# Kernel tuning notes

Hardware: AMD Instinct MI355X
Metric: run time of the kernel (lower is better)

The kernel has to match this reference:

```python
import jax, jax.numpy as jnp
import numpy as np

DIM = 4096
ROOT = 64  # int(sqrt(DIM))
B = 8192
LN_EPS = 1e-5


def setup_inputs() -> dict:
    key = jax.random.key(0)
    ks = jax.random.split(key, 7)
    return {
        "x": jax.random.normal(ks[0], (B, DIM), dtype=jnp.float32),
        "param_1": jax.random.normal(ks[1], (ROOT, 4 * ROOT, ROOT), dtype=jnp.float32),
        "bias_1": jax.random.normal(ks[2], (ROOT, 4 * ROOT), dtype=jnp.float32),
        "param_2": jax.random.normal(ks[3], (ROOT, ROOT, 4 * ROOT), dtype=jnp.float32),
        "bias_2": jax.random.normal(ks[4], (ROOT, ROOT), dtype=jnp.float32),
        "ln_gamma": jnp.ones((DIM,), dtype=jnp.float32),
        "ln_beta": jnp.zeros((DIM,), dtype=jnp.float32),
        "W": jax.random.normal(ks[5], (DIM, DIM), dtype=jnp.float32) * (1.0 / np.sqrt(DIM)),
        "b": jax.random.normal(ks[6], (DIM,), dtype=jnp.float32),
    }


def reference(x, param_1, bias_1, param_2, bias_2, ln_gamma, ln_beta, W, b):
    r = x
    # block-diagonal per-row matmuls: x -> [B, root, root]
    xb = x.reshape(-1, ROOT, ROOT)
    # fc_row: param_1[r] @ row + bias_1[r]  -> [B, root, 4*root]
    h = jnp.einsum("brk,rmk->brm", xb, param_1) + bias_1
    h = jax.nn.relu(h)
    # second per-row projection -> [B, root, root]
    h = jnp.einsum("brm,rkm->brk", h, param_2) + bias_2
    h = jax.nn.relu(h)
    h = h.reshape(-1, DIM)
    # LayerNorm (affine, eps=1e-5)
    mu = jnp.mean(h, axis=-1, keepdims=True)
    var = jnp.mean(jnp.square(h - mu), axis=-1, keepdims=True)
    h = (h - mu) * jax.lax.rsqrt(var + LN_EPS) * ln_gamma + ln_beta
    # Linear + ReLU + residual
    h = jax.nn.relu(h @ W.T + b)
    return h + r
```

## Files before the change

kernel.cpp:

```cpp
#include <hip/hip_runtime.h>

typedef __bf16 bf16;
typedef bf16 bf16x4 __attribute__((ext_vector_type(4)));
typedef bf16 bf16x8 __attribute__((ext_vector_type(8)));
typedef float floatx4 __attribute__((ext_vector_type(4)));

#define MFMA(a, b, c) __builtin_amdgcn_mfma_f32_16x16x32_bf16((a), (b), (c), 0, 0, 0)

__device__ __forceinline__ void gl2lds16(const void* g, void* l) {
  __builtin_amdgcn_global_load_lds(
      (const __attribute__((address_space(1))) void*)g,
      (__attribute__((address_space(3))) void*)l, 16, 0, 0);
}

__device__ __forceinline__ bf16x4 cvt4(const float4 v) {
  bf16x4 o;
  o[0] = (bf16)v.x; o[1] = (bf16)v.y; o[2] = (bf16)v.z; o[3] = (bf16)v.w;
  return o;
}

__global__ __launch_bounds__(256) void cast_w_kernel(const float* __restrict__ W,
                                                     bf16* __restrict__ Wb, int n4) {
  int idx = blockIdx.x * 256 + threadIdx.x;
  int stride = gridDim.x * 256;
  const float4* W4 = (const float4*)W;
  for (int i = idx; i < n4; i += stride) {
    *(bf16x4*)(Wb + (size_t)i * 4) = cvt4(W4[i]);
  }
}

__global__ __launch_bounds__(256) void blockdiag_kernel(
    const float* __restrict__ x, const float* __restrict__ p1,
    const float* __restrict__ b1, const float* __restrict__ p2,
    const float* __restrict__ b2, bf16* __restrict__ h2) {
  __shared__ bf16 sX[128 * 72];
  __shared__ bf16 sP1[64 * 72];
  __shared__ bf16 sP2[64 * 72];
  __shared__ bf16 sH1[128 * 72];
  __shared__ float sB1[256];
  __shared__ float sB2[64];

  const int tid = threadIdx.x;
  const int bt = blockIdx.x, r = blockIdx.y;
  const size_t b0 = (size_t)bt * 128;

  const float* xr = x + b0 * 4096 + r * 64;
#pragma unroll
  for (int i = 0; i < 8; ++i) {
    int idx = tid + i * 256;
    int row = idx >> 4, c4 = idx & 15;
    float4 v = *(const float4*)(xr + (size_t)row * 4096 + c4 * 4);
    *(bf16x4*)(&sX[row * 72 + c4 * 4]) = cvt4(v);
  }
  sB1[tid] = b1[r * 256 + tid];
  if (tid < 64) sB2[tid] = b2[r * 64 + tid];

  const float* p1r = p1 + (size_t)r * 16384;
  const float* p2r = p2 + (size_t)r * 16384;

  const int w = tid >> 6, lane = tid & 63;
  const int q = lane >> 4, l16 = lane & 15;
  const int wm = w >> 1, wn = w & 1;

  const floatx4 fzero = {0.f, 0.f, 0.f, 0.f};
  floatx4 acc2[4][2];
#pragma unroll
  for (int mt = 0; mt < 4; ++mt)
#pragma unroll
    for (int nt = 0; nt < 2; ++nt) acc2[mt][nt] = fzero;

  for (int qh = 0; qh < 4; ++qh) {
    __syncthreads();
#pragma unroll
    for (int i = 0; i < 4; ++i) {
      int idx = tid + i * 256;
      int row = idx >> 4, c4 = idx & 15;
      float4 v = *(const float4*)(p1r + (size_t)(qh * 64 + row) * 64 + c4 * 4);
      *(bf16x4*)(&sP1[row * 72 + c4 * 4]) = cvt4(v);
      float4 u = *(const float4*)(p2r + (size_t)row * 256 + qh * 64 + c4 * 4);
      *(bf16x4*)(&sP2[row * 72 + c4 * 4]) = cvt4(u);
    }
    __syncthreads();

    floatx4 acc1[4][2];
#pragma unroll
    for (int mt = 0; mt < 4; ++mt)
#pragma unroll
      for (int nt = 0; nt < 2; ++nt) acc1[mt][nt] = fzero;
#pragma unroll
    for (int ks = 0; ks < 2; ++ks) {
      bf16x8 a[4], bb[2];
#pragma unroll
      for (int mt = 0; mt < 4; ++mt)
        a[mt] = *(const bf16x8*)(&sX[(64 * wm + mt * 16 + l16) * 72 + ks * 32 + q * 8]);
#pragma unroll
      for (int nt = 0; nt < 2; ++nt)
        bb[nt] = *(const bf16x8*)(&sP1[(32 * wn + nt * 16 + l16) * 72 + ks * 32 + q * 8]);
#pragma unroll
      for (int mt = 0; mt < 4; ++mt)
#pragma unroll
        for (int nt = 0; nt < 2; ++nt) acc1[mt][nt] = MFMA(a[mt], bb[nt], acc1[mt][nt]);
    }
#pragma unroll
    for (int mt = 0; mt < 4; ++mt) {
#pragma unroll
      for (int nt = 0; nt < 2; ++nt) {
        int c = 32 * wn + nt * 16 + l16;
        float bias1v = sB1[qh * 64 + c];
#pragma unroll
        for (int v = 0; v < 4; ++v) {
          int row = 64 * wm + mt * 16 + q * 4 + v;
          sH1[row * 72 + c] = (bf16)fmaxf(acc1[mt][nt][v] + bias1v, 0.f);
        }
      }
    }
    __syncthreads();
#pragma unroll
    for (int ks = 0; ks < 2; ++ks) {
      bf16x8 a2[4], bb2[2];
#pragma unroll
      for (int mt = 0; mt < 4; ++mt)
        a2[mt] = *(const bf16x8*)(&sH1[(64 * wm + mt * 16 + l16) * 72 + ks * 32 + q * 8]);
#pragma unroll
      for (int nt = 0; nt < 2; ++nt)
        bb2[nt] = *(const bf16x8*)(&sP2[(32 * wn + nt * 16 + l16) * 72 + ks * 32 + q * 8]);
#pragma unroll
      for (int mt = 0; mt < 4; ++mt)
#pragma unroll
        for (int nt = 0; nt < 2; ++nt) acc2[mt][nt] = MFMA(a2[mt], bb2[nt], acc2[mt][nt]);
    }
  }

  bf16* ho = h2 + b0 * 4096 + r * 64;
#pragma unroll
  for (int mt = 0; mt < 4; ++mt) {
#pragma unroll
    for (int nt = 0; nt < 2; ++nt) {
      int kk = 32 * wn + nt * 16 + l16;
      float b2v = sB2[kk];
#pragma unroll
      for (int v = 0; v < 4; ++v) {
        int row = 64 * wm + mt * 16 + q * 4 + v;
        ho[(size_t)row * 4096 + kk] = (bf16)fmaxf(acc2[mt][nt][v] + b2v, 0.f);
      }
    }
  }
}

__global__ __launch_bounds__(256) void ln_kernel(bf16* __restrict__ h,
                                                 const float* __restrict__ gamma,
                                                 const float* __restrict__ beta) {
  const int row = blockIdx.x;
  const int tid = threadIdx.x;
  bf16* hr = h + (size_t)row * 4096;
  float vals[16];
  float s = 0.f, ss = 0.f;
#pragma unroll
  for (int i = 0; i < 2; ++i) {
    bf16x8 v = *(const bf16x8*)(hr + (size_t)(i * 256 + tid) * 8);
#pragma unroll
    for (int j = 0; j < 8; ++j) {
      float f = (float)v[j];
      vals[i * 8 + j] = f;
      s += f;
      ss += f * f;
    }
  }
#pragma unroll
  for (int off = 32; off > 0; off >>= 1) {
    s += __shfl_down(s, off, 64);
    ss += __shfl_down(ss, off, 64);
  }
  __shared__ float red[8];
  const int w = tid >> 6, lane = tid & 63;
  if (lane == 0) { red[w] = s; red[4 + w] = ss; }
  __syncthreads();
  s = red[0] + red[1] + red[2] + red[3];
  ss = red[4] + red[5] + red[6] + red[7];
  const float mu = s * (1.f / 4096.f);
  const float var = ss * (1.f / 4096.f) - mu * mu;
  const float rsig = rsqrtf(var + 1e-5f);
#pragma unroll
  for (int i = 0; i < 2; ++i) {
    const int base = (i * 256 + tid) * 8;
    float4 g0 = *(const float4*)(gamma + base);
    float4 g1 = *(const float4*)(gamma + base + 4);
    float4 be0 = *(const float4*)(beta + base);
    float4 be1 = *(const float4*)(beta + base + 4);
    float g[8] = {g0.x, g0.y, g0.z, g0.w, g1.x, g1.y, g1.z, g1.w};
    float bb[8] = {be0.x, be0.y, be0.z, be0.w, be1.x, be1.y, be1.z, be1.w};
    bf16x8 o;
#pragma unroll
    for (int j = 0; j < 8; ++j) o[j] = (bf16)((vals[i * 8 + j] - mu) * rsig * g[j] + bb[j]);
    *(bf16x8*)(hr + base) = o;
  }
}

__global__ __launch_bounds__(256) void gemm_kernel(
    const bf16* __restrict__ A,
    const bf16* __restrict__ B,
    const float* __restrict__ bias, const float* __restrict__ xres,
    float* __restrict__ out) {
  __shared__ bf16 sA[128 * 32];
  __shared__ bf16 sB[128 * 32];
  const int tid = threadIdx.x;
  const int n0 = blockIdx.x * 128;
  const int m0 = blockIdx.y * 128;
  const int w = tid >> 6, lane = tid & 63;
  const int q = lane >> 4, l16 = lane & 15;
  const int wm = w >> 1, wn = w & 1;

  const floatx4 fzero = {0.f, 0.f, 0.f, 0.f};
  floatx4 acc[4][4];
#pragma unroll
  for (int mt = 0; mt < 4; ++mt)
#pragma unroll
    for (int nt = 0; nt < 4; ++nt) acc[mt][nt] = fzero;

  const int ra = tid >> 2;
  const int koff = (tid & 3) * 8;
  const bf16* aptr = A + (size_t)(m0 + ra) * 4096 + koff;
  const bf16* bptr = B + (size_t)(n0 + ra) * 4096 + koff;
  bf16* la = sA + tid * 8;
  bf16* lb = sB + tid * 8;

  for (int k0 = 0; k0 < 4096; k0 += 32) {
    gl2lds16(aptr, la);
    gl2lds16(aptr + (size_t)64 * 4096, sA + 2048 + tid * 8);
    gl2lds16(bptr, lb);
    gl2lds16(bptr + (size_t)64 * 4096, sB + 2048 + tid * 8);
    aptr += 32;
    bptr += 32;
    __syncthreads();
    bf16x8 af[4], bfr[4];
#pragma unroll
    for (int mt = 0; mt < 4; ++mt)
      af[mt] = *(const bf16x8*)(&sA[(64 * wm + mt * 16 + l16) * 32 + q * 8]);
#pragma unroll
    for (int nt = 0; nt < 4; ++nt)
      bfr[nt] = *(const bf16x8*)(&sB[(64 * wn + nt * 16 + l16) * 32 + q * 8]);
#pragma unroll
    for (int mt = 0; mt < 4; ++mt)
#pragma unroll
      for (int nt = 0; nt < 4; ++nt) acc[mt][nt] = MFMA(af[mt], bfr[nt], acc[mt][nt]);
    __syncthreads();
  }

#pragma unroll
  for (int nt = 0; nt < 4; ++nt) {
    const int col = n0 + 64 * wn + nt * 16 + l16;
    const float bv = bias[col];
#pragma unroll
    for (int mt = 0; mt < 4; ++mt) {
#pragma unroll
      for (int v = 0; v < 4; ++v) {
        const int row = m0 + 64 * wm + mt * 16 + q * 4 + v;
        const size_t o = (size_t)row * 4096 + col;
        out[o] = fmaxf(acc[mt][nt][v] + bv, 0.f) + xres[o];
      }
    }
  }
}

extern "C" void kernel_launch(void* const* d_in, const int* in_sizes, int n_in,
                              void* d_out, int out_size, void* d_ws, size_t ws_size,
                              hipStream_t stream) {
  const float* x = (const float*)d_in[0];
  const float* p1 = (const float*)d_in[1];
  const float* b1 = (const float*)d_in[2];
  const float* p2 = (const float*)d_in[3];
  const float* b2 = (const float*)d_in[4];
  const float* gamma = (const float*)d_in[5];
  const float* beta = (const float*)d_in[6];
  const float* W = (const float*)d_in[7];
  const float* bias = (const float*)d_in[8];
  float* out = (float*)d_out;

  bf16* Wb = (bf16*)d_ws;
  bf16* h = (bf16*)((char*)d_ws + (size_t)4096 * 4096 * 2);

  cast_w_kernel<<<2048, 256, 0, stream>>>(W, Wb, 4096 * 4096 / 4);
  blockdiag_kernel<<<dim3(64, 64), 256, 0, stream>>>(x, p1, b1, p2, b2, h);
  ln_kernel<<<8192, 256, 0, stream>>>(h, gamma, beta);
  gemm_kernel<<<dim3(32, 64), 256, 0, stream>>>(h, Wb, bias, x, out);
}
```

Before: 746.9 us.

## Fold LayerNorm into GEMM epilogue, pre-cast inputs to bf16, swizzle LDS tiles

New measurement: 900.7 us. 20.6% more time.

```diff
diff --git a/kernel.cpp b/kernel.cpp
--- a/kernel.cpp
+++ b/kernel.cpp
@@ -19,23 +19,72 @@
   return o;
 }
 
-__global__ __launch_bounds__(256) void cast_w_kernel(const float* __restrict__ W,
-                                                     bf16* __restrict__ Wb, int n4) {
+__global__ __launch_bounds__(256) void castw_kernel(
+    const float* __restrict__ W, const float* __restrict__ gamma,
+    const float* __restrict__ beta, const float* __restrict__ bias,
+    bf16* __restrict__ Wb, float* __restrict__ g, float* __restrict__ cb) {
+  const int j = blockIdx.x, tid = threadIdx.x;
+  const float* wr = W + (size_t)j * 4096;
+  float wg = 0.f, wb = 0.f;
+  const int base = tid * 16;
+#pragma unroll
+  for (int i = 0; i < 4; ++i) {
+    float4 wv = *(const float4*)(wr + base + i * 4);
+    float4 gv = *(const float4*)(gamma + base + i * 4);
+    float4 bv = *(const float4*)(beta + base + i * 4);
+    float p0 = wv.x * gv.x, p1 = wv.y * gv.y, p2 = wv.z * gv.z, p3 = wv.w * gv.w;
+    bf16x4 o; o[0] = (bf16)p0; o[1] = (bf16)p1; o[2] = (bf16)p2; o[3] = (bf16)p3;
+    *(bf16x4*)(Wb + (size_t)j * 4096 + base + i * 4) = o;
+    wg += p0 + p1 + p2 + p3;
+    wb += wv.x * bv.x + wv.y * bv.y + wv.z * bv.z + wv.w * bv.w;
+  }
+#pragma unroll
+  for (int off = 32; off > 0; off >>= 1) {
+    wg += __shfl_down(wg, off, 64);
+    wb += __shfl_down(wb, off, 64);
+  }
+  __shared__ float red[8];
+  const int w = tid >> 6, lane = tid & 63;
+  if (lane == 0) { red[w] = wg; red[4 + w] = wb; }
+  __syncthreads();
+  if (tid == 0) {
+    g[j] = red[0] + red[1] + red[2] + red[3];
+    cb[j] = red[4] + red[5] + red[6] + red[7] + bias[j];
+  }
+}
+
+__global__ __launch_bounds__(256) void castx_kernel(const float* __restrict__ x,
+                                                    bf16* __restrict__ xb, int n4) {
   int idx = blockIdx.x * 256 + threadIdx.x;
   int stride = gridDim.x * 256;
-  const float4* W4 = (const float4*)W;
-  for (int i = idx; i < n4; i += stride) {
-    *(bf16x4*)(Wb + (size_t)i * 4) = cvt4(W4[i]);
+  const float4* x4 = (const float4*)x;
+  for (int i = idx; i < n4; i += stride) *(bf16x4*)(xb + (size_t)i * 4) = cvt4(x4[i]);
+}
+
+__global__ __launch_bounds__(256) void castp_kernel(const float* __restrict__ p1,
+                                                    const float* __restrict__ p2,
+                                                    bf16* __restrict__ p1b,
+                                                    bf16* __restrict__ p2b) {
+  int idx = blockIdx.x * 256 + threadIdx.x;
+  int stride = gridDim.x * 256;
+  const float4* a4 = (const float4*)p1;
+  const float4* b4 = (const float4*)p2;
+  for (int i = idx; i < 524288; i += stride) {
+    if (i < 262144) *(bf16x4*)(p1b + (size_t)i * 4) = cvt4(a4[i]);
+    else {
+      int k = i - 262144;
+      *(bf16x4*)(p2b + (size_t)k * 4) = cvt4(b4[k]);
+    }
   }
 }
 
 __global__ __launch_bounds__(256) void blockdiag_kernel(
-    const float* __restrict__ x, const float* __restrict__ p1,
-    const float* __restrict__ b1, const float* __restrict__ p2,
+    const bf16* __restrict__ xb, const bf16* __restrict__ p1b,
+    const float* __restrict__ b1, const bf16* __restrict__ p2b,
     const float* __restrict__ b2, bf16* __restrict__ h2) {
-  __shared__ bf16 sX[128 * 72];
-  __shared__ bf16 sP1[64 * 72];
-  __shared__ bf16 sP2[64 * 72];
+  __shared__ bf16 sX[128 * 64];
+  __shared__ bf16 sP1[64 * 64];
+  __shared__ bf16 sP2[64 * 64];
   __shared__ bf16 sH1[128 * 72];
   __shared__ float sB1[256];
   __shared__ float sB2[64];
@@ -44,24 +93,24 @@
   const int bt = blockIdx.x, r = blockIdx.y;
   const size_t b0 = (size_t)bt * 128;
 
-  const float* xr = x + b0 * 4096 + r * 64;
-#pragma unroll
-  for (int i = 0; i < 8; ++i) {
-    int idx = tid + i * 256;
-    int row = idx >> 4, c4 = idx & 15;
-    float4 v = *(const float4*)(xr + (size_t)row * 4096 + c4 * 4);
-    *(bf16x4*)(&sX[row * 72 + c4 * 4]) = cvt4(v);
+  const int srow = tid >> 3, ss = tid & 7;
+  const int sg = ss ^ (srow & 7);
+  {
+    const bf16* src = xb + (b0 + srow) * 4096 + r * 64 + sg * 8;
+#pragma unroll
+    for (int i = 0; i < 4; ++i)
+      gl2lds16(src + (size_t)i * 32 * 4096, sX + (tid + i * 256) * 8);
   }
   sB1[tid] = b1[r * 256 + tid];
   if (tid < 64) sB2[tid] = b2[r * 64 + tid];
-
-  const float* p1r = p1 + (size_t)r * 16384;
-  const float* p2r = p2 + (size_t)r * 16384;
 
   const int w = tid >> 6, lane = tid & 63;
   const int q = lane >> 4, l16 = lane & 15;
   const int wm = w >> 1, wn = w & 1;
 
+  const bf16* p1base = p1b + (size_t)r * 16384;
+  const bf16* p2base = p2b + (size_t)r * 16384;
+
   const floatx4 fzero = {0.f, 0.f, 0.f, 0.f};
   floatx4 acc2[4][2];
 #pragma unroll
@@ -70,17 +119,14 @@
     for (int nt = 0; nt < 2; ++nt) acc2[mt][nt] = fzero;
 
   for (int qh = 0; qh < 4; ++qh) {
+    if (qh) __syncthreads();
+#pragma unroll
+    for (int i = 0; i < 2; ++i) {
+      int row = srow + i * 32;
+      gl2lds16(p1base + (size_t)(qh * 64 + row) * 64 + sg * 8, sP1 + (tid + i * 256) * 8);
+      gl2lds16(p2base + (size_t)row * 256 + qh * 64 + sg * 8, sP2 + (tid + i * 256) * 8);
+    }
     __syncthreads();
-#pragma unroll
-    for (int i = 0; i < 4; ++i) {
-      int idx = tid + i * 256;
-      int row = idx >> 4, c4 = idx & 15;
-      float4 v = *(const float4*)(p1r + (size_t)(qh * 64 + row) * 64 + c4 * 4);
-      *(bf16x4*)(&sP1[row * 72 + c4 * 4]) = cvt4(v);
-      float4 u = *(const float4*)(p2r + (size_t)row * 256 + qh * 64 + c4 * 4);
-      *(bf16x4*)(&sP2[row * 72 + c4 * 4]) = cvt4(u);
-    }
-    __syncthreads();
 
     floatx4 acc1[4][2];
 #pragma unroll
@@ -89,13 +135,14 @@
       for (int nt = 0; nt < 2; ++nt) acc1[mt][nt] = fzero;
 #pragma unroll
     for (int ks = 0; ks < 2; ++ks) {
+      const int co = ((ks * 4 + q) ^ (l16 & 7)) * 8;
       bf16x8 a[4], bb[2];
 #pragma unroll
       for (int mt = 0; mt < 4; ++mt)
-        a[mt] = *(const bf16x8*)(&sX[(64 * wm + mt * 16 + l16) * 72 + ks * 32 + q * 8]);
+        a[mt] = *(const bf16x8*)(&sX[(64 * wm + mt * 16 + l16) * 64 + co]);
 #pragma unroll
       for (int nt = 0; nt < 2; ++nt)
-        bb[nt] = *(const bf16x8*)(&sP1[(32 * wn + nt * 16 + l16) * 72 + ks * 32 + q * 8]);
+        bb[nt] = *(const bf16x8*)(&sP1[(32 * wn + nt * 16 + l16) * 64 + co]);
 #pragma unroll
       for (int mt = 0; mt < 4; ++mt)
 #pragma unroll
@@ -115,15 +162,17 @@
       }
     }
     __syncthreads();
+
 #pragma unroll
     for (int ks = 0; ks < 2; ++ks) {
+      const int co = ((ks * 4 + q) ^ (l16 & 7)) * 8;
       bf16x8 a2[4], bb2[2];
 #pragma unroll
       for (int mt = 0; mt < 4; ++mt)
         a2[mt] = *(const bf16x8*)(&sH1[(64 * wm + mt * 16 + l16) * 72 + ks * 32 + q * 8]);
 #pragma unroll
       for (int nt = 0; nt < 2; ++nt)
-        bb2[nt] = *(const bf16x8*)(&sP2[(32 * wn + nt * 16 + l16) * 72 + ks * 32 + q * 8]);
+        bb2[nt] = *(const bf16x8*)(&sP2[(32 * wn + nt * 16 + l16) * 64 + co]);
 #pragma unroll
       for (int mt = 0; mt < 4; ++mt)
 #pragma unroll
@@ -131,29 +180,36 @@
     }
   }
 
-  bf16* ho = h2 + b0 * 4096 + r * 64;
 #pragma unroll
   for (int mt = 0; mt < 4; ++mt) {
 #pragma unroll
     for (int nt = 0; nt < 2; ++nt) {
-      int kk = 32 * wn + nt * 16 + l16;
-      float b2v = sB2[kk];
+      int col = 32 * wn + nt * 16 + l16;
+      float b2v = sB2[col];
 #pragma unroll
       for (int v = 0; v < 4; ++v) {
         int row = 64 * wm + mt * 16 + q * 4 + v;
-        ho[(size_t)row * 4096 + kk] = (bf16)fmaxf(acc2[mt][nt][v] + b2v, 0.f);
+        float val = fmaxf(acc2[mt][nt][v] + b2v, 0.f);
+        sX[row * 64 + ((col >> 3) ^ (row & 7)) * 8 + (col & 7)] = (bf16)val;
       }
     }
   }
-}
-
-__global__ __launch_bounds__(256) void ln_kernel(bf16* __restrict__ h,
-                                                 const float* __restrict__ gamma,
-                                                 const float* __restrict__ beta) {
-  const int row = blockIdx.x;
-  const int tid = threadIdx.x;
-  bf16* hr = h + (size_t)row * 4096;
-  float vals[16];
+  __syncthreads();
+  {
+    bf16* dst = h2 + (b0 + srow) * 4096 + r * 64 + sg * 8;
+#pragma unroll
+    for (int i = 0; i < 4; ++i) {
+      bf16x8 vv = *(const bf16x8*)(sX + (tid + i * 256) * 8);
+      *(bf16x8*)(dst + (size_t)i * 32 * 4096) = vv;
+    }
+  }
+}
+
+__global__ __launch_bounds__(256) void stats_kernel(const bf16* __restrict__ h,
+                                                    float* __restrict__ mu,
+                                                    float* __restrict__ rs) {
+  const int row = blockIdx.x, tid = threadIdx.x;
+  const bf16* hr = h + (size_t)row * 4096;
   float s = 0.f, ss = 0.f;
 #pragma unroll
   for (int i = 0; i < 2; ++i) {
@@ -161,9 +217,7 @@
 #pragma unroll
     for (int j = 0; j < 8; ++j) {
       float f = (float)v[j];
-      vals[i * 8 + j] = f;
-      s += f;
-      ss += f * f;
+      s += f; ss += f * f;
     }
   }
 #pragma unroll
@@ -175,34 +229,22 @@
   const int w = tid >> 6, lane = tid & 63;
   if (lane == 0) { red[w] = s; red[4 + w] = ss; }
   __syncthreads();
-  s = red[0] + red[1] + red[2] + red[3];
-  ss = red[4] + red[5] + red[6] + red[7];
-  const float mu = s * (1.f / 4096.f);
-  const float var = ss * (1.f / 4096.f) - mu * mu;
-  const float rsig = rsqrtf(var + 1e-5f);
-#pragma unroll
-  for (int i = 0; i < 2; ++i) {
-    const int base = (i * 256 + tid) * 8;
-    float4 g0 = *(const float4*)(gamma + base);
-    float4 g1 = *(const float4*)(gamma + base + 4);
-    float4 be0 = *(const float4*)(beta + base);
-    float4 be1 = *(const float4*)(beta + base + 4);
-    float g[8] = {g0.x, g0.y, g0.z, g0.w, g1.x, g1.y, g1.z, g1.w};
-    float bb[8] = {be0.x, be0.y, be0.z, be0.w, be1.x, be1.y, be1.z, be1.w};
-    bf16x8 o;
-#pragma unroll
-    for (int j = 0; j < 8; ++j) o[j] = (bf16)((vals[i * 8 + j] - mu) * rsig * g[j] + bb[j]);
-    *(bf16x8*)(hr + base) = o;
+  if (tid == 0) {
+    float st = red[0] + red[1] + red[2] + red[3];
+    float sst = red[4] + red[5] + red[6] + red[7];
+    float m = st * (1.f / 4096.f);
+    mu[row] = m;
+    rs[row] = rsqrtf(sst * (1.f / 4096.f) - m * m + 1e-5f);
   }
 }
 
 __global__ __launch_bounds__(256) void gemm_kernel(
-    const bf16* __restrict__ A,
-    const bf16* __restrict__ B,
-    const float* __restrict__ bias, const float* __restrict__ xres,
-    float* __restrict__ out) {
-  __shared__ bf16 sA[128 * 32];
-  __shared__ bf16 sB[128 * 32];
+    const bf16* __restrict__ A, const bf16* __restrict__ B,
+    const float* __restrict__ g, const float* __restrict__ cb,
+    const float* __restrict__ mu, const float* __restrict__ rs,
+    const float* __restrict__ xres, float* __restrict__ out) {
+  __shared__ bf16 sA[128 * 64];
+  __shared__ bf16 sB[128 * 64];
   const int tid = threadIdx.x;
   const int n0 = blockIdx.x * 128;
   const int m0 = blockIdx.y * 128;
@@ -217,28 +259,40 @@
 #pragma unroll
     for (int nt = 0; nt < 4; ++nt) acc[mt][nt] = fzero;
 
-  const int ra = tid >> 2;
-  const int koff = (tid & 3) * 8;
-  const bf16* aptr = A + (size_t)(m0 + ra) * 4096 + koff;
-  const bf16* bptr = B + (size_t)(n0 + ra) * 4096 + koff;
-  bf16* la = sA + tid * 8;
-  bf16* lb = sB + tid * 8;
-
-  for (int k0 = 0; k0 < 4096; k0 += 32) {
-    gl2lds16(aptr, la);
-    gl2lds16(aptr + (size_t)64 * 4096, sA + 2048 + tid * 8);
-    gl2lds16(bptr, lb);
-    gl2lds16(bptr + (size_t)64 * 4096, sB + 2048 + tid * 8);
-    aptr += 32;
-    bptr += 32;
+  const int srow = tid >> 3, ss = tid & 7;
+  const int sg = ss ^ (srow & 7);
+  const bf16* aptr = A + (size_t)(m0 + srow) * 4096 + sg * 8;
+  const bf16* bptr = B + (size_t)(n0 + srow) * 4096 + sg * 8;
+
+  const int co0 = (q ^ (l16 & 7)) * 8;
+  const int co1 = ((4 + q) ^ (l16 & 7)) * 8;
+
+  for (int k0 = 0; k0 < 4096; k0 += 64) {
+#pragma unroll
+    for (int i = 0; i < 4; ++i) {
+      gl2lds16(aptr + (size_t)i * 32 * 4096, sA + (tid + i * 256) * 8);
+      gl2lds16(bptr + (size_t)i * 32 * 4096, sB + (tid + i * 256) * 8);
+    }
+    aptr += 64;
+    bptr += 64;
     __syncthreads();
     bf16x8 af[4], bfr[4];
 #pragma unroll
     for (int mt = 0; mt < 4; ++mt)
-      af[mt] = *(const bf16x8*)(&sA[(64 * wm + mt * 16 + l16) * 32 + q * 8]);
+      af[mt] = *(const bf16x8*)(&sA[(64 * wm + mt * 16 + l16) * 64 + co0]);
 #pragma unroll
     for (int nt = 0; nt < 4; ++nt)
-      bfr[nt] = *(const bf16x8*)(&sB[(64 * wn + nt * 16 + l16) * 32 + q * 8]);
+      bfr[nt] = *(const bf16x8*)(&sB[(64 * wn + nt * 16 + l16) * 64 + co0]);
+#pragma unroll
+    for (int mt = 0; mt < 4; ++mt)
+#pragma unroll
+      for (int nt = 0; nt < 4; ++nt) acc[mt][nt] = MFMA(af[mt], bfr[nt], acc[mt][nt]);
+#pragma unroll
+    for (int mt = 0; mt < 4; ++mt)
+      af[mt] = *(const bf16x8*)(&sA[(64 * wm + mt * 16 + l16) * 64 + co1]);
+#pragma unroll
+    for (int nt = 0; nt < 4; ++nt)
+      bfr[nt] = *(const bf16x8*)(&sB[(64 * wn + nt * 16 + l16) * 64 + co1]);
 #pragma unroll
     for (int mt = 0; mt < 4; ++mt)
 #pragma unroll
@@ -246,17 +300,28 @@
     __syncthreads();
   }
 
+  float muv[16], rsv[16];
+#pragma unroll
+  for (int mt = 0; mt < 4; ++mt)
+#pragma unroll
+    for (int v = 0; v < 4; ++v) {
+      int row = m0 + 64 * wm + mt * 16 + q * 4 + v;
+      muv[mt * 4 + v] = mu[row];
+      rsv[mt * 4 + v] = rs[row];
+    }
 #pragma unroll
   for (int nt = 0; nt < 4; ++nt) {
     const int col = n0 + 64 * wn + nt * 16 + l16;
-    const float bv = bias[col];
+    const float gj = g[col];
+    const float cbj = cb[col];
 #pragma unroll
     for (int mt = 0; mt < 4; ++mt) {
 #pragma unroll
       for (int v = 0; v < 4; ++v) {
         const int row = m0 + 64 * wm + mt * 16 + q * 4 + v;
         const size_t o = (size_t)row * 4096 + col;
-        out[o] = fmaxf(acc[mt][nt][v] + bv, 0.f) + xres[o];
+        float val = rsv[mt * 4 + v] * (acc[mt][nt][v] - muv[mt * 4 + v] * gj) + cbj;
+        out[o] = fmaxf(val, 0.f) + xres[o];
       }
     }
   }
@@ -276,11 +341,21 @@
   const float* bias = (const float*)d_in[8];
   float* out = (float*)d_out;
 
+  const size_t MB = 1ull << 20;
   bf16* Wb = (bf16*)d_ws;
-  bf16* h = (bf16*)((char*)d_ws + (size_t)4096 * 4096 * 2);
-
-  cast_w_kernel<<<2048, 256, 0, stream>>>(W, Wb, 4096 * 4096 / 4);
-  blockdiag_kernel<<<dim3(64, 64), 256, 0, stream>>>(x, p1, b1, p2, b2, h);
-  ln_kernel<<<8192, 256, 0, stream>>>(h, gamma, beta);
-  gemm_kernel<<<dim3(32, 64), 256, 0, stream>>>(h, Wb, bias, x, out);
-}
+  bf16* h = (bf16*)((char*)d_ws + 32 * MB);
+  float* mu = (float*)((char*)d_ws + 96 * MB);
+  float* rs = mu + 8192;
+  float* gv = rs + 8192;
+  float* cb = gv + 4096;
+  bf16* xb = (bf16*)d_out;
+  bf16* p1b = (bf16*)((char*)d_out + 64 * MB);
+  bf16* p2b = (bf16*)((char*)d_out + 66 * MB);
+
+  castw_kernel<<<4096, 256, 0, stream>>>(W, gamma, beta, bias, Wb, gv, cb);
+  castx_kernel<<<4096, 256, 0, stream>>>(x, xb, 8192 * 4096 / 4);
+  castp_kernel<<<512, 256, 0, stream>>>(p1, p2, p1b, p2b);
+  blockdiag_kernel<<<dim3(64, 64), 256, 0, stream>>>(xb, p1b, b1, p2b, b2, h);
+  stats_kernel<<<8192, 256, 0, stream>>>(h, mu, rs);
+  gemm_kernel<<<dim3(32, 64), 256, 0, stream>>>(h, Wb, gv, cb, mu, rs, x, out);
+}
```
